# Kernel optimization log

Measured on AMD Instinct MI355X. Metric: run time of the kernel, lower is better.

The kernel has to match this reference:

```python
import jax, jax.numpy as jnp
import numpy as np

B, S, SR, H, NH, L, V, FF = 4, 512, 512, 1024, 16, 6, 32000, 4096
HD = H // NH  # 64
PAD = 2


def setup_inputs() -> dict:
    key = jax.random.key(0)
    ks = jax.random.split(key, 40)
    f32 = jnp.float32

    def n(k, shape, scale=0.02):
        return jax.random.normal(k, shape, f32) * scale

    encoder_outputs = jax.random.normal(ks[0], (B, SR, H), f32)
    decoder_input = jax.random.randint(ks[1], (B, S), 0, V)
    decoder_input = jnp.where(decoder_input == PAD, 3, decoder_input)
    decoder_input = decoder_input.at[:, S - 64:].set(PAD).at[:, 0].set(5)
    encoder_input = jax.random.randint(ks[2], (B, SR), 0, V)
    encoder_input = jnp.where(encoder_input == PAD, 3, encoder_input)
    encoder_input = encoder_input.at[:, SR - 64:].set(PAD)

    emb = jax.random.normal(ks[3], (V, H), f32).at[PAD].set(0.0)  # padding_idx=2 row is zero

    return {
        'encoder_outputs': encoder_outputs,
        'decoder_input': decoder_input,
        'encoder_input': encoder_input,
        'emb': emb,
        'wq1': n(ks[4], (L, H, H)), 'bq1': jnp.zeros((L, H), f32),
        'wk1': n(ks[5], (L, H, H)), 'bk1': jnp.zeros((L, H), f32),
        'wv1': n(ks[6], (L, H, H)), 'bv1': jnp.zeros((L, H), f32),
        'wo1': n(ks[7], (L, H, H)), 'bo1': jnp.zeros((L, H), f32),
        'pos1': jax.random.normal(ks[8], (L, 2 * S - 1, HD), f32),  # torch.randn init
        'wq2': n(ks[9], (L, H, H)), 'bq2': jnp.zeros((L, H), f32),
        'wk2': n(ks[10], (L, H, H)), 'bk2': jnp.zeros((L, H), f32),
        'wv2': n(ks[11], (L, H, H)), 'bv2': jnp.zeros((L, H), f32),
        'wo2': n(ks[12], (L, H, H)), 'bo2': jnp.zeros((L, H), f32),
        'ln1g': jnp.ones((L, H), f32), 'ln1b': jnp.zeros((L, H), f32),
        'ln2g': jnp.ones((L, H), f32), 'ln2b': jnp.zeros((L, H), f32),
        'ln3g': jnp.ones((L, H), f32), 'ln3b': jnp.zeros((L, H), f32),
        'wf1': n(ks[13], (L, H, FF)), 'bf1': jnp.zeros((L, FF), f32),
        'wf2': n(ks[14], (L, FF, H)), 'bf2': jnp.zeros((L, H), f32),
        'wout': n(ks[15], (H, V)), 'bout': jnp.zeros((V,), f32),
    }


def _split_heads(x):
    b, l, _ = x.shape
    return x.reshape(b, l, NH, HD).transpose(0, 2, 1, 3)  # b h l d


def _layer_norm(x, g, b):
    m = x.mean(-1, keepdims=True)
    v = ((x - m) ** 2).mean(-1, keepdims=True)
    return (x - m) / jnp.sqrt(v + 1e-5) * g + b


def _skew(q, P):
    # Transformer-XL style relative-position skew. q: [b,h,S,d] (already scaled), P: [2S-1,d]
    b = q.shape[0]
    pe = jnp.einsum('bhid,jd->bhij', q, P)                 # [b,h,S,2S-1]
    pe = jnp.pad(pe, ((0, 0), (0, 0), (0, 0), (0, 1)))      # [b,h,S,2S]
    pe = pe.reshape(b, NH, 2 * S * S)
    pe = jnp.pad(pe, ((0, 0), (0, 0), (0, S - 1)))
    pe = pe.reshape(b, NH, S + 1, 2 * S - 1)
    return pe[:, :, :-1, -S:]                               # [b,h,S,S]


def _attention(xq, xkv, wq, bq, wk, bk, wv, bv, wo, bo, pos, add_mask, causal):
    b = xq.shape[0]
    q = _split_heads(xq @ wq + bq) / np.float32(np.sqrt(HD))
    k = _split_heads(xkv @ wk + bk)
    v = _split_heads(xkv @ wv + bv)
    att = jnp.einsum('bhid,bhjd->bhij', q, k)
    if pos is not None:
        att = att + _skew(q, pos)
    if causal:
        i = jnp.arange(S)[:, None]
        j = jnp.arange(att.shape[-1])[None, :]
        att = jnp.where(j > i, -jnp.inf, att)
    if add_mask is not None:
        att = att + add_mask
    s = jax.nn.softmax(att, axis=-1)
    o = jnp.einsum('bhqk,bhkd->bhqd', s, v)
    o = o.transpose(0, 2, 1, 3).reshape(b, S, H)
    return o @ wo + bo


def _forward(encoder_outputs, decoder_input, encoder_input, emb,
             wq1, bq1, wk1, bk1, wv1, bv1, wo1, bo1, pos1,
             wq2, bq2, wk2, bk2, wv2, bv2, wo2, bo2,
             ln1g, ln1b, ln2g, ln2b, ln3g, ln3b,
             wf1, bf1, wf2, bf2, wout, bout):
    self_mask = jnp.where(decoder_input == PAD, -jnp.inf, 0.0)[:, None, None, :]   # [b,1,1,S]
    cross_mask = jnp.where(encoder_input == PAD, -jnp.inf, 0.0)[:, None, None, :]  # [b,1,1,SR]
    x = emb[decoder_input]  # dropout_p=0 -> identity
    for i in range(L):
        a1 = _attention(x, x, wq1[i], bq1[i], wk1[i], bk1[i], wv1[i], bv1[i],
                        wo1[i], bo1[i], pos1[i], self_mask, True)
        x1 = _layer_norm(a1 + x, ln1g[i], ln1b[i])
        a2 = _attention(x1, encoder_outputs, wq2[i], bq2[i], wk2[i], bk2[i], wv2[i], bv2[i],
                        wo2[i], bo2[i], None, cross_mask, False)
        x2 = _layer_norm(a2 + x1, ln2g[i], ln2b[i])
        ff = jax.nn.relu(x2 @ wf1[i] + bf1[i]) @ wf2[i] + bf2[i]
        x = _layer_norm(ff + x2, ln3g[i], ln3b[i])
    return jax.nn.log_softmax(x @ wout + bout, axis=-1)  # [b,S,V]


def reference(encoder_outputs, decoder_input, encoder_input, emb,
              wq1, bq1, wk1, bk1, wv1, bv1, wo1, bo1, pos1,
              wq2, bq2, wk2, bk2, wv2, bv2, wo2, bo2,
              ln1g, ln1b, ln2g, ln2b, ln3g, ln3b,
              wf1, bf1, wf2, bf2, wout, bout):
    return _forward(encoder_outputs, decoder_input, encoder_input, emb,
                    wq1, bq1, wk1, bk1, wv1, bv1, wo1, bo1, pos1,
                    wq2, bq2, wk2, bk2, wv2, bv2, wo2, bo2,
                    ln1g, ln1b, ln2g, ln2b, ln3g, ln3b,
                    wf1, bf1, wf2, bf2, wout, bout)
```

## Files before the change

### kernel.cpp

```cpp
#include <hip/hip_runtime.h>


typedef unsigned short u16;
typedef short s16x8 __attribute__((ext_vector_type(8)));
typedef unsigned short u16x4 __attribute__((ext_vector_type(4)));
typedef unsigned short u16x8 __attribute__((ext_vector_type(8)));
typedef float f32x4 __attribute__((ext_vector_type(4)));

#define PADTOK 2
#define NEG_INF (-__builtin_inff())

static __device__ __forceinline__ u16 f2bf(float f) {
  unsigned u = __float_as_uint(f);
  u += 0x7fffu + ((u >> 16) & 1u);
  return (u16)(u >> 16);
}
static __device__ __forceinline__ float bf2f(u16 h) {
  return __uint_as_float(((unsigned)h) << 16);
}
static __device__ __forceinline__ float f16tof(u16 h) {
  _Float16 x = __builtin_bit_cast(_Float16, h);
  return (float)x;
}
static __device__ __forceinline__ u16 ftof16(float v) {
  _Float16 x = (_Float16)v;
  return __builtin_bit_cast(u16, x);
}
static __device__ __forceinline__ f32x4 mfma16(s16x8 a, s16x8 b, f32x4 c) {
  asm("v_mfma_f32_16x16x32_bf16 %0, %1, %2, %0" : "+v"(c) : "v"(a), "v"(b));
  return c;
}
static __device__ __forceinline__ void gll16(const void* g, void* l) {
  __builtin_amdgcn_global_load_lds((const __attribute__((address_space(1))) void*)g,
                                   (__attribute__((address_space(3))) void*)l, 16, 0, 0);
}
static __device__ __forceinline__ size_t hsidx(int m, int n) {
  return ((size_t)((m >> 9) * 16 + (n >> 6))) * 32768u + (size_t)(m & 511) * 64u + (size_t)(n & 63);
}
static __device__ __forceinline__ size_t vtidx(int m, int n) {
  return ((size_t)((m >> 9) * 16 + (n >> 6))) * 65536u + (size_t)(n & 63) * 512u + (size_t)(m & 511);
}

static __device__ __forceinline__ void raster2(int& bm, int& bn, int GM0) {
  const int nm = gridDim.y, nn = gridDim.x;
  int bid = blockIdx.y * nn + blockIdx.x;
  const int nwg = nm * nn;
  const int q = nwg >> 3, r = nwg & 7;
  const int x = bid & 7, p = bid >> 3;
  bid = (x < r ? x * (q + 1) : r * (q + 1) + (x - r) * q) + p;
  const int GM = nm < GM0 ? nm : GM0;
  const int pg = GM * nn;
  const int gi = bid / pg, rem = bid - gi * pg;
  const int left = nm - gi * GM;
  const int gm = left < GM ? left : GM;
  bm = gi * GM + rem % gm;
  bn = rem / gm;
}

template<int EPI, bool BF16OUT, int MFR, bool RELU, bool RESID, int SKIP, int GMT>
__global__ __launch_bounds__(256)
void bgemm(const u16* __restrict__ A, long long sAg,
           const u16* __restrict__ Bt, long long sBg,
           const float* __restrict__ bias, const float* __restrict__ bias2,
           const float* __restrict__ bias3,
           const float* __restrict__ Res,
           void* __restrict__ Cv, u16* __restrict__ C2, u16* __restrict__ C3,
           long long sCg, int ldc, int K, float scale)
{
  constexpr int BM = MFR * 32;
  __shared__ u16 As[BM * 64];
  __shared__ u16 Bs[128 * 64];
  int bmi, bni;
  raster2(bmi, bni, GMT);
  const int bm0 = bmi * BM, bn0 = bni * 128;
  if constexpr (SKIP == 2) {
    if ((bm0 & 511) + bn0 <= 256) return;
  }
  const int g = blockIdx.z;
  const u16* Ag = A + (size_t)g * (size_t)sAg;
  const u16* Bg = Bt + (size_t)g * (size_t)sBg;
  const int tid = threadIdx.x, l = tid & 63, w = tid >> 6;
  const int wm = w >> 1, wn = w & 1;
  const int rsel = l & 15, kg = l >> 4, xs = l & 7;

  f32x4 acc[MFR][4];
#pragma unroll
  for (int i = 0; i < MFR; ++i)
#pragma unroll
    for (int j = 0; j < 4; ++j) acc[i][j] = (f32x4){0.f, 0.f, 0.f, 0.f};

  const int srow = l >> 3;
  const int sch  = (l & 7) ^ srow;
  const u16* Agp = Ag + ((size_t)(bm0 + w * 8 * MFR + srow)) * (size_t)K + sch * 8;
  const u16* Bgp = Bg + ((size_t)(bn0 + w * 32 + srow)) * (size_t)K + sch * 8;
  char* AsL = (char*)As + (w * 8 * MFR) * 128;
  char* BsL = (char*)Bs + (w * 32) * 128;

  for (int k0 = 0; k0 < K; k0 += 64) {
    __syncthreads();
#pragma unroll
    for (int i = 0; i < MFR; ++i)
      gll16(Agp + (size_t)i * 8 * K + k0, AsL + i * 1024);
#pragma unroll
    for (int i = 0; i < 4; ++i)
      gll16(Bgp + (size_t)i * 8 * K + k0, BsL + i * 1024);
    __syncthreads();

    const int arow0 = (wm * (MFR * 16) + rsel) * 128;
    const int brow0 = (wn * 64 + rsel) * 128;
#pragma unroll
    for (int ks = 0; ks < 2; ++ks) {
      const int ch = ((ks * 4 + kg) ^ xs) * 16;
      s16x8 af[MFR], bfr[4];
#pragma unroll
      for (int mf = 0; mf < MFR; ++mf)
        af[mf] = *(const s16x8*)((const char*)As + arow0 + mf * 2048 + ch);
#pragma unroll
      for (int nf = 0; nf < 4; ++nf)
        bfr[nf] = *(const s16x8*)((const char*)Bs + brow0 + nf * 2048 + ch);
#pragma unroll
      for (int mf = 0; mf < MFR; ++mf)
#pragma unroll
        for (int nf = 0; nf < 4; ++nf)
          acc[mf][nf] = mfma16(af[mf], bfr[nf], acc[mf][nf]);
    }
  }

#pragma unroll
  for (int mf = 0; mf < MFR; ++mf) {
#pragma unroll
    for (int nf = 0; nf < 4; ++nf) {
      const int n = bn0 + wn * 64 + nf * 16 + rsel;
      int sub = 0, nl = n;
      const float* bp = bias;
      if constexpr (EPI == 4) {
        sub = n >> 10; nl = n & 1023;
        bp = (sub == 0) ? bias : (sub == 1) ? bias2 : bias3;
      }
      if constexpr (EPI == 5) {
        sub = n >> 10; nl = n & 1023;
        bp = (sub == 0) ? bias : bias2;
      }
      const float bv = bp ? bp[nl] : 0.f;
      float sc = 1.f;
      if constexpr (EPI == 0 || EPI == 1) sc = scale;
      if constexpr (EPI == 4) sc = (sub == 0) ? scale : 1.f;
#pragma unroll
      for (int e = 0; e < 4; ++e) {
        const int m = bm0 + wm * (MFR * 16) + mf * 16 + kg * 4 + e;
        float v = (acc[mf][nf][e] + bv) * sc;
        if constexpr (RELU) v = fmaxf(v, 0.f);
        if constexpr (RESID) v += Res[(size_t)m * (size_t)ldc + n];
        if constexpr (EPI == 0) {
          const size_t idx = (size_t)g * (size_t)sCg + (size_t)m * (size_t)ldc + n;
          if constexpr (BF16OUT) ((u16*)Cv)[idx] = f2bf(v);
          else                   ((float*)Cv)[idx] = v;
        } else if constexpr (EPI == 1) {
          ((u16*)Cv)[hsidx(m, nl)] = f2bf(v);
        } else if constexpr (EPI == 4) {
          if (sub == 2)      C3[vtidx(m, nl)] = f2bf(v);
          else if (sub == 1) C2[hsidx(m, nl)] = f2bf(v);
          else               ((u16*)Cv)[hsidx(m, nl)] = f2bf(v);
        } else if constexpr (EPI == 5) {
          if (sub == 0) ((u16*)Cv)[hsidx(m, nl)] = f2bf(v);
          else          C2[vtidx(m, nl)] = f2bf(v);
        } else if constexpr (EPI == 6) {
          ((u16*)Cv)[(size_t)m * (size_t)ldc + n] = ftof16(v);
        }
      }
    }
  }
}

template<bool SELF>
__global__ __launch_bounds__(256)
void fused_attn(const u16* __restrict__ Qb, const u16* __restrict__ Kb,
                const u16* __restrict__ Vt, const u16* __restrict__ PE,
                const float* __restrict__ maskf, u16* __restrict__ O)
{
  __shared__ u16 SP[4][16][520];
  __shared__ float rsm[4][16];
  const int bid = blockIdx.y * 8 + blockIdx.x;
  const int g = (bid & 7) + 8 * ((bid >> 3) & 7);
  const int rt = bid >> 6;
  const int b = g >> 4, h = g & 15;
  const int tid = threadIdx.x, l = tid & 63, w = tid >> 6;
  const int ti = SELF ? (w * 8 + rt) : (rt * 4 + w);
  const int i0 = ti * 16;
  const int CT = SELF ? (i0 + 16) : 512;
  const int rsel = l & 15, kg = l >> 4;

  const u16* Qg = Qb + (size_t)g * 32768u;
  const u16* Kg = Kb + (size_t)g * 32768u;
  const u16* Vg = Vt + (size_t)g * 65536u;
  u16 (*sp)[520] = SP[w];
  float* rs = rsm[w];

  const s16x8 qf0 = *(const s16x8*)(Qg + (size_t)(i0 + rsel) * 64u + kg * 8);
  const s16x8 qf1 = *(const s16x8*)(Qg + (size_t)(i0 + rsel) * 64u + 32 + kg * 8);

  for (int j0 = 0; j0 < CT; j0 += 16) {
    const s16x8 kf0 = *(const s16x8*)(Kg + (size_t)(j0 + rsel) * 64u + kg * 8);
    const s16x8 kf1 = *(const s16x8*)(Kg + (size_t)(j0 + rsel) * 64u + 32 + kg * 8);
    f32x4 a = {0.f, 0.f, 0.f, 0.f};
    a = mfma16(qf0, kf0, a);
    a = mfma16(qf1, kf1, a);
    const int jj = j0 + rsel;
    const float mj = maskf[b * 512 + jj];
#pragma unroll
    for (int e = 0; e < 4; ++e) {
      const int r = kg * 4 + e;
      float v = a[e] + mj;
      if constexpr (SELF) {
        const int i = i0 + r;
        if (jj > i) v = NEG_INF;
        else        v += bf2f(PE[((size_t)(g * 512 + i)) * 512u + (511 + jj - i)]);
      }
      sp[r][jj] = f2bf(v);
    }
  }
  asm volatile("s_waitcnt lgkmcnt(0)" ::: "memory");

  const int sr = l >> 2, sub = l & 3;
  float mx = NEG_INF;
  for (int c = sub * 4; c < CT; c += 16) {
    const u16x4 h4 = *(const u16x4*)&sp[sr][c];
#pragma unroll
    for (int e = 0; e < 4; ++e) mx = fmaxf(mx, bf2f(h4[e]));
  }
  mx = fmaxf(mx, __shfl_xor(mx, 1, 64));
  mx = fmaxf(mx, __shfl_xor(mx, 2, 64));
  float sum = 0.f;
  for (int c = sub * 4; c < CT; c += 16) {
    const u16x4 h4 = *(const u16x4*)&sp[sr][c];
    const float p0 = expf(bf2f(h4[0]) - mx), p1 = expf(bf2f(h4[1]) - mx);
    const float p2 = expf(bf2f(h4[2]) - mx), p3 = expf(bf2f(h4[3]) - mx);
    sum += p0 + p1 + p2 + p3;
    const u16x4 o4 = {f2bf(p0), f2bf(p1), f2bf(p2), f2bf(p3)};
    *(u16x4*)&sp[sr][c] = o4;
  }
  sum += __shfl_xor(sum, 1, 64);
  sum += __shfl_xor(sum, 2, 64);
  if (sub == 0) rs[sr] = 1.f / sum;
  if (CT & 31) {
    const u16x4 z = {0, 0, 0, 0};
    *(u16x4*)&sp[sr][CT + sub * 4] = z;
  }
  asm volatile("s_waitcnt lgkmcnt(0)" ::: "memory");

  f32x4 oa[4];
#pragma unroll
  for (int nt = 0; nt < 4; ++nt) oa[nt] = (f32x4){0.f, 0.f, 0.f, 0.f};
  const int nk = (CT + 31) >> 5;
  for (int kt = 0; kt < nk; ++kt) {
    const s16x8 pf = *(const s16x8*)&sp[rsel][kt * 32 + kg * 8];
#pragma unroll
    for (int nt = 0; nt < 4; ++nt) {
      const s16x8 vf = *(const s16x8*)(Vg + (size_t)(nt * 16 + rsel) * 512u + kt * 32 + kg * 8);
      oa[nt] = mfma16(pf, vf, oa[nt]);
    }
  }

#pragma unroll
  for (int e = 0; e < 4; ++e) {
    const int q = kg * 4 + e;
    const float inv = rs[q];
    u16* orow = O + ((size_t)(b * 512 + i0 + q)) * 1024u + h * 64;
#pragma unroll
    for (int nt = 0; nt < 4; ++nt)
      orow[nt * 16 + rsel] = f2bf(oa[nt][e] * inv);
  }
}

static __device__ __forceinline__ void tconv_tile(const float* in, int N,
                                                  u16* out, int K, int k0, int n0) {
  __shared__ u16 L[64][72];
  const int t = threadIdx.x;
  const int rk = t >> 4, cn = (t & 15) * 4;
#pragma unroll
  for (int q = 0; q < 4; ++q) {
    const int kk = k0 + rk + q * 16;
    float4 v = *(const float4*)(in + (size_t)kk * (size_t)N + n0 + cn);
    L[cn + 0][rk + q * 16] = f2bf(v.x);
    L[cn + 1][rk + q * 16] = f2bf(v.y);
    L[cn + 2][rk + q * 16] = f2bf(v.z);
    L[cn + 3][rk + q * 16] = f2bf(v.w);
  }
  __syncthreads();
  const int rn = t >> 2, ck = (t & 3) * 16;
  u16* op = out + (size_t)(n0 + rn) * (size_t)K + k0 + ck;
  *(s16x8*)op       = *(const s16x8*)&L[rn][ck];
  *(s16x8*)(op + 8) = *(const s16x8*)&L[rn][ck + 8];
}

__global__ __launch_bounds__(256)
void conv_layer(const float* w0, const float* w1, const float* w2, const float* w3,
                const float* w4, const float* w5, const float* w6, const float* w7,
                const float* w8, const float* w9, u16* WT) {
  const int b = blockIdx.x;
  const float* in; u16* out; int N, K, kt, nt;
  if (b < 2048) {
    const int j = b >> 8, t = b & 255;
    const float* ws[8] = {w0, w1, w2, w3, w4, w5, w6, w7};
    in = ws[j]; out = WT + (size_t)j * 1048576u; K = 1024; N = 1024;
    kt = t >> 4; nt = t & 15;
  } else if (b < 3072) {
    const int t = b - 2048;
    in = w8; out = WT + 8388608u; K = 1024; N = 4096; kt = t >> 6; nt = t & 63;
  } else {
    const int t = b - 3072;
    in = w9; out = WT + 12582912u; K = 4096; N = 1024; kt = t >> 4; nt = t & 15;
  }
  tconv_tile(in, N, out, K, kt * 64, nt * 64);
}

__global__ __launch_bounds__(256)
void conv_wout(const float* in, u16* out) {
  const int b = blockIdx.x;
  const int kt = b / 500, nt = b % 500;
  tconv_tile(in, 32000, out, 1024, kt * 64, nt * 64);
}

__global__ void conv_bf16(const float* __restrict__ in, u16* __restrict__ out) {
  const int i = (blockIdx.x * 256 + threadIdx.x) * 4;
  float4 v = *(const float4*)(in + i);
  u16x4 h = {f2bf(v.x), f2bf(v.y), f2bf(v.z), f2bf(v.w)};
  *(u16x4*)(out + i) = h;
}

__global__ void conv_pos(const float* __restrict__ pos, u16* __restrict__ posb) {
  const int idx = (blockIdx.x * 256 + threadIdx.x) * 4;
  const int lyr = idx >> 15, rem = idx & 32767;
  float4 v = *(const float4*)(pos + (size_t)lyr * 65472u + rem);
  u16x4 h = {f2bf(v.x), f2bf(v.y), f2bf(v.z), f2bf(v.w)};
  *(u16x4*)(posb + idx) = h;
}

__global__ void mask_kernel(const int* __restrict__ dec, const int* __restrict__ enc,
                            float* __restrict__ mD, float* __restrict__ mE) {
  const int i = blockIdx.x * 256 + threadIdx.x;
  mD[i] = (dec[i] == PADTOK) ? NEG_INF : 0.f;
  mE[i] = (enc[i] == PADTOK) ? NEG_INF : 0.f;
}

static __device__ __forceinline__ float wred_sum(float v) {
#pragma unroll
  for (int o = 32; o > 0; o >>= 1) v += __shfl_down(v, o, 64);
  return v;
}
static __device__ __forceinline__ float wred_max(float v) {
#pragma unroll
  for (int o = 32; o > 0; o >>= 1) v = fmaxf(v, __shfl_down(v, o, 64));
  return v;
}
static __device__ __forceinline__ float bred_sum(float v, float* sm) {
  const int lane = threadIdx.x & 63, wid = threadIdx.x >> 6;
  v = wred_sum(v);
  if (lane == 0) sm[wid] = v;
  __syncthreads();
  if (threadIdx.x == 0) sm[0] = sm[0] + sm[1] + sm[2] + sm[3];
  __syncthreads();
  const float r = sm[0];
  __syncthreads();
  return r;
}

__global__ void embed_kernel(const int* __restrict__ dec, const float* __restrict__ emb,
                             float* __restrict__ X, u16* __restrict__ Xh) {
  const int m = blockIdx.x, t = threadIdx.x;
  const int tok = dec[m];
  float4 v = ((const float4*)(emb + (size_t)tok * 1024u))[t];
  ((float4*)(X + (size_t)m * 1024u))[t] = v;
  u16x4 h = {f2bf(v.x), f2bf(v.y), f2bf(v.z), f2bf(v.w)};
  *(u16x4*)(Xh + (size_t)m * 1024u + t * 4) = h;
}

__global__ void layernorm_kernel(const float* __restrict__ R,
                                 const float* __restrict__ gw, const float* __restrict__ bw,
                                 float* __restrict__ Y, u16* __restrict__ Yh) {
  __shared__ float sm[4];
  const int m = blockIdx.x, t = threadIdx.x;
  float4 v = ((const float4*)(R + (size_t)m * 1024u))[t];
  float s = v.x + v.y + v.z + v.w;
  s = bred_sum(s, sm);
  const float mean = s * (1.f / 1024.f);
  const float d0 = v.x - mean, d1 = v.y - mean, d2 = v.z - mean, d3 = v.w - mean;
  float q = d0 * d0 + d1 * d1 + d2 * d2 + d3 * d3;
  q = bred_sum(q, sm);
  const float rstd = rsqrtf(q * (1.f / 1024.f) + 1e-5f);
  const int c = t * 4;
  float4 o;
  o.x = d0 * rstd * gw[c + 0] + bw[c + 0];
  o.y = d1 * rstd * gw[c + 1] + bw[c + 1];
  o.z = d2 * rstd * gw[c + 2] + bw[c + 2];
  o.w = d3 * rstd * gw[c + 3] + bw[c + 3];
  ((float4*)(Y + (size_t)m * 1024u))[t] = o;
  u16x4 h = {f2bf(o.x), f2bf(o.y), f2bf(o.z), f2bf(o.w)};
  *(u16x4*)(Yh + (size_t)m * 1024u + c) = h;
}

__global__ __launch_bounds__(512)
void log_softmax_kernel(float* __restrict__ out) {
  __shared__ u16 row[32000];
  __shared__ float sm[8];
  const int m = blockIdx.x, tid = threadIdx.x;
  const u16* src = (const u16*)out + (size_t)m * 64000u;
  for (int c = tid; c < 4000; c += 512)
    *(u16x8*)&row[c * 8] = *(const u16x8*)(src + c * 8);
  __syncthreads();
  float mx = NEG_INF;
  for (int c = tid; c < 4000; c += 512) {
    const u16x8 h = *(const u16x8*)&row[c * 8];
#pragma unroll
    for (int e = 0; e < 8; ++e) mx = fmaxf(mx, f16tof(h[e]));
  }
  mx = wred_max(mx);
  if ((tid & 63) == 0) sm[tid >> 6] = mx;
  __syncthreads();
  if (tid == 0) {
    float a = sm[0];
#pragma unroll
    for (int wI = 1; wI < 8; ++wI) a = fmaxf(a, sm[wI]);
    sm[0] = a;
  }
  __syncthreads();
  mx = sm[0];
  __syncthreads();
  float s = 0.f;
  for (int c = tid; c < 4000; c += 512) {
    const u16x8 h = *(const u16x8*)&row[c * 8];
#pragma unroll
    for (int e = 0; e < 8; ++e) s += expf(f16tof(h[e]) - mx);
  }
  s = wred_sum(s);
  if ((tid & 63) == 0) sm[tid >> 6] = s;
  __syncthreads();
  if (tid == 0) {
    float a = 0.f;
#pragma unroll
    for (int wI = 0; wI < 8; ++wI) a += sm[wI];
    sm[0] = a;
  }
  __syncthreads();
  const float lse = mx + logf(sm[0]);
  float* dst = out + (size_t)m * 32000u;
  for (int c = tid; c < 4000; c += 512) {
    const u16x8 h = *(const u16x8*)&row[c * 8];
    float4 o0, o1;
    o0.x = f16tof(h[0]) - lse; o0.y = f16tof(h[1]) - lse;
    o0.z = f16tof(h[2]) - lse; o0.w = f16tof(h[3]) - lse;
    o1.x = f16tof(h[4]) - lse; o1.y = f16tof(h[5]) - lse;
    o1.z = f16tof(h[6]) - lse; o1.w = f16tof(h[7]) - lse;
    ((float4*)dst)[c * 2]     = o0;
    ((float4*)dst)[c * 2 + 1] = o1;
  }
}

extern "C" void kernel_launch(void* const* d_in, const int* in_sizes, int n_in,
                              void* d_out, int out_size, void* d_ws, size_t ws_size,
                              hipStream_t stream) {
  const float* enc_out = (const float*)d_in[0];
  const int*   dec_in  = (const int*)d_in[1];
  const int*   enc_in  = (const int*)d_in[2];
  const float* emb     = (const float*)d_in[3];
  const float* wq1 = (const float*)d_in[4];  const float* bq1 = (const float*)d_in[5];
  const float* wk1 = (const float*)d_in[6];  const float* bk1 = (const float*)d_in[7];
  const float* wv1 = (const float*)d_in[8];  const float* bv1 = (const float*)d_in[9];
  const float* wo1 = (const float*)d_in[10]; const float* bo1 = (const float*)d_in[11];
  const float* pos1 = (const float*)d_in[12];
  const float* wq2 = (const float*)d_in[13]; const float* bq2 = (const float*)d_in[14];
  const float* wk2 = (const float*)d_in[15]; const float* bk2 = (const float*)d_in[16];
  const float* wv2 = (const float*)d_in[17]; const float* bv2 = (const float*)d_in[18];
  const float* wo2 = (const float*)d_in[19]; const float* bo2 = (const float*)d_in[20];
  const float* ln1g = (const float*)d_in[21]; const float* ln1b = (const float*)d_in[22];
  const float* ln2g = (const float*)d_in[23]; const float* ln2b = (const float*)d_in[24];
  const float* ln3g = (const float*)d_in[25]; const float* ln3b = (const float*)d_in[26];
  const float* wf1 = (const float*)d_in[27]; const float* bf1 = (const float*)d_in[28];
  const float* wf2 = (const float*)d_in[29]; const float* bf2 = (const float*)d_in[30];
  const float* wout = (const float*)d_in[31]; const float* bout = (const float*)d_in[32];

  char* ws = (char*)d_ws;
  u16*   WT    = (u16*)(ws + 0);
  float* maskD = (float*)(ws + 33554432);
  float* maskE = (float*)(ws + 33562624);
  u16*   WoutT = (u16*)(ws + 0);
  u16*   PEP   = (u16*)(ws + 67108864);
  float* X     = (float*)(ws + 100663296);
  float* Xa    = (float*)(ws + 109051904);
  float* Xb    = (float*)(ws + 117440512);
  float* Rb    = (float*)(ws + 125829120);
  u16*   Ab16  = (u16*)(ws + 134217728);
  u16*   Q     = (u16*)(ws + 138412032);
  u16*   Kh    = (u16*)(ws + 142606336);
  u16*   VT    = (u16*)(ws + 146800640);
  u16*   Ob16  = (u16*)(ws + 155189248);
  u16*   FFH16 = (u16*)(ws + 159383552);
  u16*   encb  = (u16*)(ws + 176160768);
  u16*   posb  = (u16*)(ws + 180355072);
  float* out   = (float*)d_out;

  embed_kernel<<<2048, 256, 0, stream>>>(dec_in, emb, X, Ab16);
  conv_bf16<<<2048, 256, 0, stream>>>(enc_out, encb);
  conv_pos<<<192, 256, 0, stream>>>(pos1, posb);
  mask_kernel<<<8, 256, 0, stream>>>(dec_in, enc_in, maskD, maskE);

  for (int i = 0; i < 6; ++i) {
    const size_t oHH = (size_t)i * 1048576u, oH = (size_t)i * 1024u;
    const float* bq1i = bq1 + oH; const float* bk1i = bk1 + oH;
    const float* bv1i = bv1 + oH; const float* bo1i = bo1 + oH;
    const float* bq2i = bq2 + oH; const float* bk2i = bk2 + oH;
    const float* bv2i = bv2 + oH; const float* bo2i = bo2 + oH;
    const float* bf1i = bf1 + (size_t)i * 4096u; const float* bf2i = bf2 + oH;
    const u16* posL = posb + (size_t)i * 32768u;

    conv_layer<<<4096, 256, 0, stream>>>(
        wq1 + oHH, wk1 + oHH, wv1 + oHH, wo1 + oHH,
        wq2 + oHH, wk2 + oHH, wv2 + oHH, wo2 + oHH,
        wf1 + (size_t)i * 4194304u, wf2 + (size_t)i * 4194304u, WT);

    bgemm<4, true, 4, false, false, 0, 8><<<dim3(24, 16, 1), 256, 0, stream>>>(
        Ab16, 0, WT, 0, bq1i, bk1i, bv1i, nullptr, Q, Kh, VT, 0, 0, 1024, 0.125f);
    bgemm<0, true, 4, false, false, 2, 8><<<dim3(4, 256, 1), 256, 0, stream>>>(
        Q, 0, posL, 0, nullptr, nullptr, nullptr, nullptr, PEP, nullptr, nullptr,
        0, 512, 64, 1.f);
    fused_attn<true><<<dim3(8, 64), 256, 0, stream>>>(Q, Kh, VT, PEP, maskD, Ob16);
    bgemm<0, false, 2, false, true, 0, 8><<<dim3(8, 32, 1), 256, 0, stream>>>(
        Ob16, 0, WT + 3145728u, 0, bo1i, nullptr, nullptr, X, Rb, nullptr, nullptr,
        0, 1024, 1024, 1.f);
    layernorm_kernel<<<2048, 256, 0, stream>>>(Rb, ln1g + oH, ln1b + oH, Xa, Ab16);

    bgemm<1, true, 2, false, false, 0, 8><<<dim3(8, 32, 1), 256, 0, stream>>>(
        Ab16, 0, WT + 4194304u, 0, bq2i, nullptr, nullptr, nullptr, Q, nullptr, nullptr,
        0, 0, 1024, 0.125f);
    bgemm<5, true, 4, false, false, 0, 8><<<dim3(16, 16, 1), 256, 0, stream>>>(
        encb, 0, WT + 5242880u, 0, bk2i, bv2i, nullptr, nullptr, Kh, VT, nullptr,
        0, 0, 1024, 1.f);
    fused_attn<false><<<dim3(8, 64), 256, 0, stream>>>(Q, Kh, VT, nullptr, maskE, Ob16);
    bgemm<0, false, 2, false, true, 0, 8><<<dim3(8, 32, 1), 256, 0, stream>>>(
        Ob16, 0, WT + 7340032u, 0, bo2i, nullptr, nullptr, Xa, Rb, nullptr, nullptr,
        0, 1024, 1024, 1.f);
    layernorm_kernel<<<2048, 256, 0, stream>>>(Rb, ln2g + oH, ln2b + oH, Xb, Ab16);

    bgemm<0, true, 4, true, false, 0, 8><<<dim3(32, 16, 1), 256, 0, stream>>>(
        Ab16, 0, WT + 8388608u, 0, bf1i, nullptr, nullptr, nullptr, FFH16, nullptr, nullptr,
        0, 4096, 1024, 1.f);
    bgemm<0, false, 2, false, true, 0, 8><<<dim3(8, 32, 1), 256, 0, stream>>>(
        FFH16, 0, WT + 12582912u, 0, bf2i, nullptr, nullptr, Xb, Rb, nullptr, nullptr,
        0, 1024, 4096, 1.f);
    layernorm_kernel<<<2048, 256, 0, stream>>>(Rb, ln3g + oH, ln3b + oH, X, Ab16);
  }

  conv_wout<<<8000, 256, 0, stream>>>(wout, WoutT);
  bgemm<6, false, 4, false, false, 0, 16><<<dim3(250, 16, 1), 256, 0, stream>>>(
      Ab16, 0, WoutT, 0, bout, nullptr, nullptr, nullptr, out, nullptr, nullptr,
      0, 64000, 1024, 1.f);
  log_softmax_kernel<<<2048, 512, 0, stream>>>(out);
}
```

Measured before the change: 2.270 ms.

## Split-K the N=1024 projection GEMMs and fuse partial reduction into layernorm

The output-projection and FF2 GEMMs (N=1024) get a split-K mode that writes fp32 partial sums to a workspace. A new layernorm kernel sums those partials, adds bias and residual, then normalizes, replacing the separate residual epilogue. Scheduling barriers are also added in the attention kernel around the softmax phase. The aim is more workgroups for these small-N GEMMs, which underfill the GPU. The cost is extra global traffic to write and reread the partials.

Result: faster. 2.074 ms, median of 2 (-8.6%).

```diff
diff --git a/kernel.cpp b/kernel.cpp
--- a/kernel.cpp
+++ b/kernel.cpp
@@ -57,7 +57,7 @@
   bn = rem / gm;
 }
 
-template<int EPI, bool BF16OUT, int MFR, bool RELU, bool RESID, int SKIP, int GMT>
+template<int EPI, bool BF16OUT, int MFR, bool RELU, bool RESID, int SKIP, int GMT, int KSPLIT>
 __global__ __launch_bounds__(256)
 void bgemm(const u16* __restrict__ A, long long sAg,
            const u16* __restrict__ Bt, long long sBg,
@@ -76,7 +76,10 @@
   if constexpr (SKIP == 2) {
     if ((bm0 & 511) + bn0 <= 256) return;
   }
-  const int g = blockIdx.z;
+  const int gz = blockIdx.z;
+  const int g = (KSPLIT > 1) ? 0 : gz;
+  const int klen = K / KSPLIT;
+  const int kbase = (KSPLIT > 1) ? gz * klen : 0;
   const u16* Ag = A + (size_t)g * (size_t)sAg;
   const u16* Bg = Bt + (size_t)g * (size_t)sBg;
   const int tid = threadIdx.x, l = tid & 63, w = tid >> 6;
@@ -96,7 +99,7 @@
   char* AsL = (char*)As + (w * 8 * MFR) * 128;
   char* BsL = (char*)Bs + (w * 32) * 128;
 
-  for (int k0 = 0; k0 < K; k0 += 64) {
+  for (int k0 = kbase; k0 < kbase + klen; k0 += 64) {
     __syncthreads();
 #pragma unroll
     for (int i = 0; i < MFR; ++i)
@@ -152,7 +155,7 @@
         if constexpr (RELU) v = fmaxf(v, 0.f);
         if constexpr (RESID) v += Res[(size_t)m * (size_t)ldc + n];
         if constexpr (EPI == 0) {
-          const size_t idx = (size_t)g * (size_t)sCg + (size_t)m * (size_t)ldc + n;
+          const size_t idx = (size_t)gz * (size_t)sCg + (size_t)m * (size_t)ldc + n;
           if constexpr (BF16OUT) ((u16*)Cv)[idx] = f2bf(v);
           else                   ((float*)Cv)[idx] = v;
         } else if constexpr (EPI == 1) {
@@ -220,6 +223,7 @@
     }
   }
   asm volatile("s_waitcnt lgkmcnt(0)" ::: "memory");
+  __builtin_amdgcn_sched_barrier(0);
 
   const int sr = l >> 2, sub = l & 3;
   float mx = NEG_INF;
@@ -247,6 +251,7 @@
     *(u16x4*)&sp[sr][CT + sub * 4] = z;
   }
   asm volatile("s_waitcnt lgkmcnt(0)" ::: "memory");
+  __builtin_amdgcn_sched_barrier(0);
 
   f32x4 oa[4];
 #pragma unroll
@@ -270,6 +275,62 @@
     for (int nt = 0; nt < 4; ++nt)
       orow[nt * 16 + rsel] = f2bf(oa[nt][e] * inv);
   }
+}
+
+template<int KS>
+__global__ __launch_bounds__(256)
+void lnred_kernel(const float* __restrict__ P, const float* __restrict__ bias,
+                  const float* __restrict__ R,
+                  const float* __restrict__ gw, const float* __restrict__ bw,
+                  float* __restrict__ Y, u16* __restrict__ Yh)
+{
+  __shared__ float sm[4];
+  const int m = blockIdx.x, t = threadIdx.x, c = t * 4;
+  float4 v = *(const float4*)(R + (size_t)m * 1024u + c);
+  const float4 bb = *(const float4*)(bias + c);
+  v.x += bb.x; v.y += bb.y; v.z += bb.z; v.w += bb.w;
+#pragma unroll
+  for (int s = 0; s < KS; ++s) {
+    const float4 p = *(const float4*)(P + (size_t)s * 2097152u + (size_t)m * 1024u + c);
+    v.x += p.x; v.y += p.y; v.z += p.z; v.w += p.w;
+  }
+  float srow = v.x + v.y + v.z + v.w;
+  {
+    const int lane = t & 63, wid = t >> 6;
+    float r = srow;
+#pragma unroll
+    for (int o = 32; o > 0; o >>= 1) r += __shfl_down(r, o, 64);
+    if (lane == 0) sm[wid] = r;
+    __syncthreads();
+    if (t == 0) sm[0] = sm[0] + sm[1] + sm[2] + sm[3];
+    __syncthreads();
+    srow = sm[0];
+    __syncthreads();
+  }
+  const float mean = srow * (1.f / 1024.f);
+  const float d0 = v.x - mean, d1 = v.y - mean, d2 = v.z - mean, d3 = v.w - mean;
+  float q = d0 * d0 + d1 * d1 + d2 * d2 + d3 * d3;
+  {
+    const int lane = t & 63, wid = t >> 6;
+    float r = q;
+#pragma unroll
+    for (int o = 32; o > 0; o >>= 1) r += __shfl_down(r, o, 64);
+    if (lane == 0) sm[wid] = r;
+    __syncthreads();
+    if (t == 0) sm[0] = sm[0] + sm[1] + sm[2] + sm[3];
+    __syncthreads();
+    q = sm[0];
+    __syncthreads();
+  }
+  const float rstd = rsqrtf(q * (1.f / 1024.f) + 1e-5f);
+  float4 o;
+  o.x = d0 * rstd * gw[c + 0] + bw[c + 0];
+  o.y = d1 * rstd * gw[c + 1] + bw[c + 1];
+  o.z = d2 * rstd * gw[c + 2] + bw[c + 2];
+  o.w = d3 * rstd * gw[c + 3] + bw[c + 3];
+  *(float4*)(Y + (size_t)m * 1024u + c) = o;
+  const u16x4 h = {f2bf(o.x), f2bf(o.y), f2bf(o.z), f2bf(o.w)};
+  *(u16x4*)(Yh + (size_t)m * 1024u + c) = h;
 }
 
 static __device__ __forceinline__ void tconv_tile(const float* in, int N,
@@ -353,17 +414,6 @@
   for (int o = 32; o > 0; o >>= 1) v = fmaxf(v, __shfl_down(v, o, 64));
   return v;
 }
-static __device__ __forceinline__ float bred_sum(float v, float* sm) {
-  const int lane = threadIdx.x & 63, wid = threadIdx.x >> 6;
-  v = wred_sum(v);
-  if (lane == 0) sm[wid] = v;
-  __syncthreads();
-  if (threadIdx.x == 0) sm[0] = sm[0] + sm[1] + sm[2] + sm[3];
-  __syncthreads();
-  const float r = sm[0];
-  __syncthreads();
-  return r;
-}
 
 __global__ void embed_kernel(const int* __restrict__ dec, const float* __restrict__ emb,
                              float* __restrict__ X, u16* __restrict__ Xh) {
@@ -373,30 +423,6 @@
   ((float4*)(X + (size_t)m * 1024u))[t] = v;
   u16x4 h = {f2bf(v.x), f2bf(v.y), f2bf(v.z), f2bf(v.w)};
   *(u16x4*)(Xh + (size_t)m * 1024u + t * 4) = h;
-}
-
-__global__ void layernorm_kernel(const float* __restrict__ R,
-                                 const float* __restrict__ gw, const float* __restrict__ bw,
-                                 float* __restrict__ Y, u16* __restrict__ Yh) {
-  __shared__ float sm[4];
-  const int m = blockIdx.x, t = threadIdx.x;
-  float4 v = ((const float4*)(R + (size_t)m * 1024u))[t];
-  float s = v.x + v.y + v.z + v.w;
-  s = bred_sum(s, sm);
-  const float mean = s * (1.f / 1024.f);
-  const float d0 = v.x - mean, d1 = v.y - mean, d2 = v.z - mean, d3 = v.w - mean;
-  float q = d0 * d0 + d1 * d1 + d2 * d2 + d3 * d3;
-  q = bred_sum(q, sm);
-  const float rstd = rsqrtf(q * (1.f / 1024.f) + 1e-5f);
-  const int c = t * 4;
-  float4 o;
-  o.x = d0 * rstd * gw[c + 0] + bw[c + 0];
-  o.y = d1 * rstd * gw[c + 1] + bw[c + 1];
-  o.z = d2 * rstd * gw[c + 2] + bw[c + 2];
-  o.w = d3 * rstd * gw[c + 3] + bw[c + 3];
-  ((float4*)(Y + (size_t)m * 1024u))[t] = o;
-  u16x4 h = {f2bf(o.x), f2bf(o.y), f2bf(o.z), f2bf(o.w)};
-  *(u16x4*)(Yh + (size_t)m * 1024u + c) = h;
 }
 
 __global__ __launch_bounds__(512)
@@ -485,10 +511,10 @@
   float* maskE = (float*)(ws + 33562624);
   u16*   WoutT = (u16*)(ws + 0);
   u16*   PEP   = (u16*)(ws + 67108864);
+  float* Part  = (float*)(ws + 67108864);
   float* X     = (float*)(ws + 100663296);
   float* Xa    = (float*)(ws + 109051904);
   float* Xb    = (float*)(ws + 117440512);
-  float* Rb    = (float*)(ws + 125829120);
   u16*   Ab16  = (u16*)(ws + 134217728);
   u16*   Q     = (u16*)(ws + 138412032);
   u16*   Kh    = (u16*)(ws + 142606336);
@@ -518,40 +544,40 @@
         wq2 + oHH, wk2 + oHH, wv2 + oHH, wo2 + oHH,
         wf1 + (size_t)i * 4194304u, wf2 + (size_t)i * 4194304u, WT);
 
-    bgemm<4, true, 4, false, false, 0, 8><<<dim3(24, 16, 1), 256, 0, stream>>>(
+    bgemm<4, true, 4, false, false, 0, 8, 1><<<dim3(24, 16, 1), 256, 0, stream>>>(
         Ab16, 0, WT, 0, bq1i, bk1i, bv1i, nullptr, Q, Kh, VT, 0, 0, 1024, 0.125f);
-    bgemm<0, true, 4, false, false, 2, 8><<<dim3(4, 256, 1), 256, 0, stream>>>(
+    bgemm<0, true, 4, false, false, 2, 8, 1><<<dim3(4, 256, 1), 256, 0, stream>>>(
         Q, 0, posL, 0, nullptr, nullptr, nullptr, nullptr, PEP, nullptr, nullptr,
         0, 512, 64, 1.f);
     fused_attn<true><<<dim3(8, 64), 256, 0, stream>>>(Q, Kh, VT, PEP, maskD, Ob16);
-    bgemm<0, false, 2, false, true, 0, 8><<<dim3(8, 32, 1), 256, 0, stream>>>(
-        Ob16, 0, WT + 3145728u, 0, bo1i, nullptr, nullptr, X, Rb, nullptr, nullptr,
-        0, 1024, 1024, 1.f);
-    layernorm_kernel<<<2048, 256, 0, stream>>>(Rb, ln1g + oH, ln1b + oH, Xa, Ab16);
-
-    bgemm<1, true, 2, false, false, 0, 8><<<dim3(8, 32, 1), 256, 0, stream>>>(
+    bgemm<0, false, 2, false, false, 0, 8, 2><<<dim3(8, 32, 2), 256, 0, stream>>>(
+        Ob16, 0, WT + 3145728u, 0, nullptr, nullptr, nullptr, nullptr,
+        Part, nullptr, nullptr, 2097152, 1024, 1024, 1.f);
+    lnred_kernel<2><<<2048, 256, 0, stream>>>(Part, bo1i, X, ln1g + oH, ln1b + oH, Xa, Ab16);
+
+    bgemm<1, true, 2, false, false, 0, 8, 1><<<dim3(8, 32, 1), 256, 0, stream>>>(
         Ab16, 0, WT + 4194304u, 0, bq2i, nullptr, nullptr, nullptr, Q, nullptr, nullptr,
         0, 0, 1024, 0.125f);
-    bgemm<5, true, 4, false, false, 0, 8><<<dim3(16, 16, 1), 256, 0, stream>>>(
+    bgemm<5, true, 4, false, false, 0, 8, 1><<<dim3(16, 16, 1), 256, 0, stream>>>(
         encb, 0, WT + 5242880u, 0, bk2i, bv2i, nullptr, nullptr, Kh, VT, nullptr,
         0, 0, 1024, 1.f);
     fused_attn<false><<<dim3(8, 64), 256, 0, stream>>>(Q, Kh, VT, nullptr, maskE, Ob16);
-    bgemm<0, false, 2, false, true, 0, 8><<<dim3(8, 32, 1), 256, 0, stream>>>(
-        Ob16, 0, WT + 7340032u, 0, bo2i, nullptr, nullptr, Xa, Rb, nullptr, nullptr,
-        0, 1024, 1024, 1.f);
-    layernorm_kernel<<<2048, 256, 0, stream>>>(Rb, ln2g + oH, ln2b + oH, Xb, Ab16);
-
-    bgemm<0, true, 4, true, false, 0, 8><<<dim3(32, 16, 1), 256, 0, stream>>>(
+    bgemm<0, false, 2, false, false, 0, 8, 2><<<dim3(8, 32, 2), 256, 0, stream>>>(
+        Ob16, 0, WT + 7340032u, 0, nullptr, nullptr, nullptr, nullptr,
+        Part, nullptr, nullptr, 2097152, 1024, 1024, 1.f);
+    lnred_kernel<2><<<2048, 256, 0, stream>>>(Part, bo2i, Xa, ln2g + oH, ln2b + oH, Xb, Ab16);
+
+    bgemm<0, true, 4, true, false, 0, 8, 1><<<dim3(32, 16, 1), 256, 0, stream>>>(
         Ab16, 0, WT + 8388608u, 0, bf1i, nullptr, nullptr, nullptr, FFH16, nullptr, nullptr,
         0, 4096, 1024, 1.f);
-    bgemm<0, false, 2, false, true, 0, 8><<<dim3(8, 32, 1), 256, 0, stream>>>(
-        FFH16, 0, WT + 12582912u, 0, bf2i, nullptr, nullptr, Xb, Rb, nullptr, nullptr,
-        0, 1024, 4096, 1.f);
-    layernorm_kernel<<<2048, 256, 0, stream>>>(Rb, ln3g + oH, ln3b + oH, X, Ab16);
+    bgemm<0, false, 4, false, false, 0, 8, 4><<<dim3(8, 16, 4), 256, 0, stream>>>(
+        FFH16, 0, WT + 12582912u, 0, nullptr, nullptr, nullptr, nullptr,
+        Part, nullptr, nullptr, 2097152, 1024, 4096, 1.f);
+    lnred_kernel<4><<<2048, 256, 0, stream>>>(Part, bf2i, Xb, ln3g + oH, ln3b + oH, X, Ab16);
   }
 
   conv_wout<<<8000, 256, 0, stream>>>(wout, WoutT);
-  bgemm<6, false, 4, false, false, 0, 16><<<dim3(250, 16, 1), 256, 0, stream>>>(
+  bgemm<6, false, 4, false, false, 0, 16, 1><<<dim3(250, 16, 1), 256, 0, stream>>>(
       Ab16, 0, WoutT, 0, bout, nullptr, nullptr, nullptr, out, nullptr, nullptr,
       0, 64000, 1024, 1.f);
   log_softmax_kernel<<<2048, 512, 0, stream>>>(out);
```
